# Kernel optimization log

Measured on AMD Instinct MI355X. Metric: run time of the kernel, lower is better.

The kernel has to match this reference:

```python
import jax, jax.numpy as jnp
import numpy as np

H_FEATS = 256

def setup_inputs() -> dict:
    key = jax.random.key(0)
    k1, k2, k3, k4, k5, k6, k7 = jax.random.split(key, 7)
    N, E, D = 100000, 500000, H_FEATS
    h = jax.random.normal(k1, (N, D), dtype=jnp.float32)
    src = jax.random.randint(k2, (E,), 0, N)
    dst = jax.random.randint(k3, (E,), 0, N)
    # Linear params (PyTorch default init: U(-1/sqrt(fan_in), 1/sqrt(fan_in)))
    b1_bound = 1.0 / np.sqrt(2 * D)
    b2_bound = 1.0 / np.sqrt(D)
    W1 = jax.random.uniform(k4, (2 * D, D), jnp.float32, -b1_bound, b1_bound)
    b1 = jax.random.uniform(k5, (D,), jnp.float32, -b1_bound, b1_bound)
    W2 = jax.random.uniform(k6, (D, 1), jnp.float32, -b2_bound, b2_bound)
    b2 = jax.random.uniform(k7, (1,), jnp.float32, -b2_bound, b2_bound)
    return {"h": h, "src": src, "dst": dst, "W1": W1, "b1": b1, "W2": W2, "b2": b2}

def reference(h, src, dst, W1, b1, W2, b2):
    # Gather per-edge source/destination node features and concat: [E, 2D]
    he = jnp.concatenate([h[src], h[dst]], axis=1)
    # Linear -> ReLU -> (dropout is identity in eval) -> Linear -> Sigmoid
    hid = jax.nn.relu(he @ W1 + b1)          # [E, D]
    score = jax.nn.sigmoid((hid @ W2 + b2).squeeze(1))  # [E]
    return score
```

## Files before the change

kernel.cpp:

```cpp
#include <hip/hip_runtime.h>
#include <math.h>


typedef __attribute__((ext_vector_type(8))) short short8;
typedef __attribute__((ext_vector_type(2))) float floatx2;
typedef __attribute__((ext_vector_type(4))) float floatx4;
typedef __attribute__((ext_vector_type(16))) float floatx16;

#define D_FEAT 256
#define EPW 16

__device__ __forceinline__ float bf2f(unsigned short u) {
    union { unsigned u32; float f; } v; v.u32 = ((unsigned)u) << 16; return v.f;
}
__device__ __forceinline__ float lo16(unsigned u) {
    union { unsigned u32; float f; } v; v.u32 = u << 16; return v.f;
}
__device__ __forceinline__ float hi16(unsigned u) {
    union { unsigned u32; float f; } v; v.u32 = u & 0xffff0000u; return v.f;
}
__device__ __forceinline__ unsigned short f2bf(float f) {
    union { float f; unsigned u32; } v; v.f = f;
    unsigned x = v.u32;
    return (unsigned short)((x + 0x7fffu + ((x >> 16) & 1u)) >> 16);
}
__device__ __forceinline__ float sigmoid_safe(float r) {
    r = fminf(fmaxf(r, -30.f), 30.f);
    return 1.f / (1.f + expf(-r));
}
__device__ __forceinline__ unsigned pack4_fp8(float a, float b, float c, float d) {
    int w = __builtin_amdgcn_cvt_pk_fp8_f32(a, b, 0, false);
    w = __builtin_amdgcn_cvt_pk_fp8_f32(c, d, w, true);
    return (unsigned)w;
}

__global__ __launch_bounds__(256) void probe_dtype(const unsigned short* __restrict__ h,
                                                   int* __restrict__ flag) {
    __shared__ int cnt[256];
    const int t = threadIdx.x;
    int c = 0;
    #pragma unroll
    for (int i = 0; i < 8; ++i) {
        unsigned e = (h[t * 8 + i] >> 7) & 0xFF;
        c += (e >= 100 && e <= 140) ? 1 : 0;
    }
    cnt[t] = c;
    __syncthreads();
    if (t == 0) {
        int s = 0;
        for (int i = 0; i < 256; ++i) s += cnt[i];
        flag[0] = (s >= 1843) ? 1 : 0;
    }
}

template <int MODE>
__global__ __launch_bounds__(256) void build_wt_t(const void* __restrict__ W1v,
                                                  unsigned short* __restrict__ Wt,
                                                  const int* __restrict__ flag) {
    if (flag[0] != MODE) return;
    int j = blockIdx.x, k = threadIdx.x;
    size_t idx = (j < 256) ? ((size_t)k * 256 + j) : ((size_t)(k + 256) * 256 + (j - 256));
    unsigned short v;
    if constexpr (MODE == 1) v = ((const unsigned short*)W1v)[idx];
    else                     v = f2bf(((const float*)W1v)[idx]);
    Wt[(size_t)j * 256 + k] = v;
}

template <int MODE>
__global__ __launch_bounds__(512, 2) void gemm_pq_t(const void* __restrict__ hv,
                                                    const unsigned short* __restrict__ Wt,
                                                    unsigned char* __restrict__ PQ8,
                                                    int N, const int* __restrict__ flag) {
    if (flag[0] != MODE) return;
    __shared__ unsigned short Bs[256][256];
    __shared__ unsigned short As[64][256];

    const int tid  = threadIdx.x;
    const int lane = tid & 63;
    const int wid  = tid >> 6;
    const int l32  = lane & 31;
    const int q2   = lane >> 5;

    {
        const int r = tid >> 1;
        const unsigned cbase = (tid & 1) * 256;
        const char* srcp = (const char*)Wt + (size_t)r * 512 + cbase;
        char* dstb = (char*)&Bs[0][0] + (unsigned)r * 512;
        const unsigned sw = ((unsigned)r & 31) << 4;
        #pragma unroll
        for (int i = 0; i < 16; ++i) {
            short8 v = *(const short8*)(srcp + i * 16);
            *(short8*)(dstb + ((cbase + i * 16) ^ sw)) = v;
        }
    }

    short8 breg[16];
    {
        const char* bp = (const char*)Wt + (size_t)(256 + wid * 32 + l32) * 512 + q2 * 16;
        #pragma unroll
        for (int ks = 0; ks < 16; ++ks)
            breg[ks] = *(const short8*)(bp + ks * 32);
    }

    const int ar = tid >> 3;
    const unsigned ac = (unsigned)(tid & 7) * 64;
    const unsigned aswz = ((unsigned)ar & 31) << 4;

    short8  pref[4];
    floatx4 pf[8];
    auto load_a = [&](int ms) {
        const int gm = ms * 64 + ar;
        if constexpr (MODE == 1) {
            #pragma unroll
            for (int j = 0; j < 4; ++j) {
                short8 v = {};
                if (gm < N)
                    v = *(const short8*)((const char*)hv + (size_t)gm * 512 + ac + j * 16);
                pref[j] = v;
            }
        } else {
            #pragma unroll
            for (int j = 0; j < 4; ++j) {
                floatx4 f0 = {}, f1 = {};
                if (gm < N) {
                    const float* p = (const float*)hv + (size_t)gm * 256 + (ac + j * 16) / 2;
                    f0 = *(const floatx4*)p;
                    f1 = *(const floatx4*)(p + 4);
                }
                pf[2 * j]     = f0;
                pf[2 * j + 1] = f1;
            }
        }
    };

    const int NT = (N + 63) >> 6;
    const int GM = gridDim.x;
    if ((int)blockIdx.x < NT) load_a(blockIdx.x);

    for (int ms = blockIdx.x; ms < NT; ms += GM) {
        __syncthreads();
        {
            char* adst = (char*)&As[0][0] + (unsigned)ar * 512;
            #pragma unroll
            for (int j = 0; j < 4; ++j) {
                short8 v;
                if constexpr (MODE == 1) {
                    v = pref[j];
                } else {
                    floatx4 f0 = pf[2 * j], f1 = pf[2 * j + 1];
                    v[0] = (short)f2bf(f0.x); v[1] = (short)f2bf(f0.y);
                    v[2] = (short)f2bf(f0.z); v[3] = (short)f2bf(f0.w);
                    v[4] = (short)f2bf(f1.x); v[5] = (short)f2bf(f1.y);
                    v[6] = (short)f2bf(f1.z); v[7] = (short)f2bf(f1.w);
                }
                *(short8*)(adst + ((ac + j * 16) ^ aswz)) = v;
            }
        }
        const int msn = ms + GM;
        if (msn < NT) load_a(msn);
        __syncthreads();

        floatx16 acc[2][2] = {};
        #pragma unroll
        for (int ks = 0; ks < 16; ++ks) {
            const unsigned cb = ((unsigned)(ks * 32 + q2 * 16)) ^ ((unsigned)l32 << 4);
            short8 a0 = *(const short8*)((const char*)&As[0][0] + (unsigned)l32 * 512 + cb);
            short8 a1 = *(const short8*)((const char*)&As[0][0] + (unsigned)(32 + l32) * 512 + cb);
            short8 bl = *(const short8*)((const char*)&Bs[0][0] + (unsigned)(wid * 32 + l32) * 512 + cb);
            acc[0][0] = __builtin_amdgcn_mfma_f32_32x32x16_bf16(bl,       a0, acc[0][0], 0, 0, 0);
            acc[1][0] = __builtin_amdgcn_mfma_f32_32x32x16_bf16(bl,       a1, acc[1][0], 0, 0, 0);
            acc[0][1] = __builtin_amdgcn_mfma_f32_32x32x16_bf16(breg[ks], a0, acc[0][1], 0, 0, 0);
            acc[1][1] = __builtin_amdgcn_mfma_f32_32x32x16_bf16(breg[ks], a1, acc[1][1], 0, 0, 0);
        }

        __syncthreads();
        {
            unsigned char* scr = (unsigned char*)&As[0][0];
            #pragma unroll
            for (int mi = 0; mi < 2; ++mi) {
                const unsigned row = (unsigned)(mi * 32 + l32);
                const unsigned rs = (row & 31) << 4;
                #pragma unroll
                for (int nb = 0; nb < 2; ++nb) {
                    const unsigned nbase = (unsigned)(nb * 256 + wid * 32 + 4 * q2);
                    #pragma unroll
                    for (int g = 0; g < 4; ++g) {
                        unsigned w = pack4_fp8(acc[mi][nb][4 * g + 0], acc[mi][nb][4 * g + 1],
                                               acc[mi][nb][4 * g + 2], acc[mi][nb][4 * g + 3]);
                        const unsigned col = nbase + 8 * g;
                        *(unsigned*)(scr + ((row * 512 + col) ^ rs)) = w;
                    }
                }
            }
        }
        __syncthreads();
        {
            const unsigned char* scr = (const unsigned char*)&As[0][0];
            const int gm = ms * 64 + ar;
            if (gm < N) {
                #pragma unroll
                for (int j = 0; j < 4; ++j) {
                    const unsigned col = ac + j * 16;
                    uint4 v = *(const uint4*)(scr + (((unsigned)ar * 512 + col) ^ aswz));
                    *(uint4*)(PQ8 + (size_t)gm * 512 + col) = v;
                }
            }
        }
    }
}

template <int MODE>
__global__ __launch_bounds__(256) void edge_score_t(const unsigned char* __restrict__ PQ8,
                                                    const int* __restrict__ src,
                                                    const int* __restrict__ dst,
                                                    const void* __restrict__ b1v,
                                                    const void* __restrict__ W2v,
                                                    const void* __restrict__ b2v,
                                                    void* __restrict__ outv,
                                                    int E, const int* __restrict__ flag) {
    if (flag[0] != MODE) return;
    const int wave = threadIdx.x >> 6;
    const int lane = threadIdx.x & 63;
    const int e0 = (blockIdx.x * 4 + wave) * EPW;
    if (e0 >= E) return;
    const int l32 = lane & 31;
    const int par = lane >> 5;

    float bf[8], wf[8];
    if constexpr (MODE == 1) {
        const uint4 bvr = *(const uint4*)((const unsigned short*)b1v + l32 * 8);
        const uint4 wvr = *(const uint4*)((const unsigned short*)W2v + l32 * 8);
        bf[0] = lo16(bvr.x); bf[1] = hi16(bvr.x); bf[2] = lo16(bvr.y); bf[3] = hi16(bvr.y);
        bf[4] = lo16(bvr.z); bf[5] = hi16(bvr.z); bf[6] = lo16(bvr.w); bf[7] = hi16(bvr.w);
        wf[0] = lo16(wvr.x); wf[1] = hi16(wvr.x); wf[2] = lo16(wvr.y); wf[3] = hi16(wvr.y);
        wf[4] = lo16(wvr.z); wf[5] = hi16(wvr.z); wf[6] = lo16(wvr.w); wf[7] = hi16(wvr.w);
    } else {
        const float* bp = (const float*)b1v + l32 * 8;
        const float* wp = (const float*)W2v + l32 * 8;
        #pragma unroll
        for (int t = 0; t < 8; ++t) { bf[t] = bp[t]; wf[t] = wp[t]; }
    }
    float bias2;
    if constexpr (MODE == 1) bias2 = bf2f(((const unsigned short*)b2v)[0]);
    else                     bias2 = ((const float*)b2v)[0];

    int nsrc[8], ndst[8];
    #pragma unroll
    for (int p = 0; p < 8; ++p) {
        int e = e0 + 2 * p + par; if (e >= E) e = E - 1;
        nsrc[p] = src[e];
        ndst[p] = dst[e];
    }
    uint2 rp[8], rq[8];
    #pragma unroll
    for (int p = 0; p < 8; ++p) {
        rp[p] = *(const uint2*)(PQ8 + (size_t)nsrc[p] * 512 + l32 * 8);
        rq[p] = *(const uint2*)(PQ8 + (size_t)ndst[p] * 512 + 256 + l32 * 8);
    }

    float res[8];
    #pragma unroll
    for (int p = 0; p < 8; ++p) {
        floatx2 p01 = __builtin_amdgcn_cvt_pk_f32_fp8((int)rp[p].x, false);
        floatx2 p23 = __builtin_amdgcn_cvt_pk_f32_fp8((int)rp[p].x, true);
        floatx2 p45 = __builtin_amdgcn_cvt_pk_f32_fp8((int)rp[p].y, false);
        floatx2 p67 = __builtin_amdgcn_cvt_pk_f32_fp8((int)rp[p].y, true);
        floatx2 q01 = __builtin_amdgcn_cvt_pk_f32_fp8((int)rq[p].x, false);
        floatx2 q23 = __builtin_amdgcn_cvt_pk_f32_fp8((int)rq[p].x, true);
        floatx2 q45 = __builtin_amdgcn_cvt_pk_f32_fp8((int)rq[p].y, false);
        floatx2 q67 = __builtin_amdgcn_cvt_pk_f32_fp8((int)rq[p].y, true);
        float v0 = fmaxf(p01.x + q01.x + bf[0], 0.f);
        float v1 = fmaxf(p01.y + q01.y + bf[1], 0.f);
        float v2 = fmaxf(p23.x + q23.x + bf[2], 0.f);
        float v3 = fmaxf(p23.y + q23.y + bf[3], 0.f);
        float v4 = fmaxf(p45.x + q45.x + bf[4], 0.f);
        float v5 = fmaxf(p45.y + q45.y + bf[5], 0.f);
        float v6 = fmaxf(p67.x + q67.x + bf[6], 0.f);
        float v7 = fmaxf(p67.y + q67.y + bf[7], 0.f);
        res[p] = v0 * wf[0] + v1 * wf[1] + v2 * wf[2] + v3 * wf[3]
               + v4 * wf[4] + v5 * wf[5] + v6 * wf[6] + v7 * wf[7];
    }

    float t4[4];
    #pragma unroll
    for (int k = 0; k < 4; ++k) {
        float a = res[2 * k], b = res[2 * k + 1];
        float own  = (lane & 1) ? b : a;
        float send = (lane & 1) ? a : b;
        t4[k] = own + __shfl_xor(send, 1);
    }
    float t2[2];
    #pragma unroll
    for (int k = 0; k < 2; ++k) {
        float a = t4[2 * k], b = t4[2 * k + 1];
        float own  = (lane & 2) ? b : a;
        float send = (lane & 2) ? a : b;
        t2[k] = own + __shfl_xor(send, 2);
    }
    float t1;
    {
        float a = t2[0], b = t2[1];
        float own  = (lane & 4) ? b : a;
        float send = (lane & 4) ? a : b;
        t1 = own + __shfl_xor(send, 4);
    }
    t1 += __shfl_xor(t1, 8);
    t1 += __shfl_xor(t1, 16);

    if (l32 < 8) {
        const int e = e0 + 2 * (lane & 7) + par;
        if (e < E) {
            float r = sigmoid_safe(t1 + bias2);
            if constexpr (MODE == 1) ((unsigned short*)outv)[e] = f2bf(r);
            else                     ((float*)outv)[e] = r;
        }
    }
}

template <int MODE>
__global__ __launch_bounds__(256) void edge_fused_t(const void* __restrict__ hv,
                                                    const int* __restrict__ src,
                                                    const int* __restrict__ dst,
                                                    const void* __restrict__ W1v,
                                                    const void* __restrict__ b1v,
                                                    const void* __restrict__ W2v,
                                                    const void* __restrict__ b2v,
                                                    void* __restrict__ outv,
                                                    int E, const int* __restrict__ flag) {
    if (flag && flag[0] != MODE) return;
    __shared__ float he[512];
    __shared__ float wsum[4];
    const int e = blockIdx.x;
    if (e >= E) return;
    const int t = threadIdx.x;
    const int s = src[e];
    const int d = dst[e];

    if constexpr (MODE == 1) {
        he[t]       = bf2f(((const unsigned short*)hv)[(size_t)s * 256 + t]);
        he[256 + t] = bf2f(((const unsigned short*)hv)[(size_t)d * 256 + t]);
    } else {
        he[t]       = ((const float*)hv)[(size_t)s * 256 + t];
        he[256 + t] = ((const float*)hv)[(size_t)d * 256 + t];
    }
    __syncthreads();

    float acc;
    if constexpr (MODE == 1) acc = bf2f(((const unsigned short*)b1v)[t]);
    else                     acc = ((const float*)b1v)[t];

    #pragma unroll 8
    for (int k = 0; k < 512; ++k) {
        float w;
        if constexpr (MODE == 1) w = bf2f(((const unsigned short*)W1v)[(size_t)k * 256 + t]);
        else                     w = ((const float*)W1v)[(size_t)k * 256 + t];
        acc += he[k] * w;
    }

    float w2;
    if constexpr (MODE == 1) w2 = bf2f(((const unsigned short*)W2v)[t]);
    else                     w2 = ((const float*)W2v)[t];
    acc = fmaxf(acc, 0.f) * w2;

    #pragma unroll
    for (int off = 32; off > 0; off >>= 1)
        acc += __shfl_xor(acc, off);
    if ((t & 63) == 0) wsum[t >> 6] = acc;
    __syncthreads();

    if (t == 0) {
        float bias2;
        if constexpr (MODE == 1) bias2 = bf2f(((const unsigned short*)b2v)[0]);
        else                     bias2 = ((const float*)b2v)[0];
        float r = sigmoid_safe(wsum[0] + wsum[1] + wsum[2] + wsum[3] + bias2);
        if constexpr (MODE == 1) ((unsigned short*)outv)[e] = f2bf(r);
        else                     ((float*)outv)[e] = r;
    }
}

extern "C" void kernel_launch(void* const* d_in, const int* in_sizes, int n_in,
                              void* d_out, int out_size, void* d_ws, size_t ws_size,
                              hipStream_t stream) {
    const void* h  = d_in[0];
    const int* src = (const int*)d_in[1];
    const int* dst = (const int*)d_in[2];
    const void* W1 = d_in[3];
    const void* b1 = d_in[4];
    const void* W2 = d_in[5];
    const void* b2 = d_in[6];

    const int N = in_sizes[0] / D_FEAT;
    const int E = in_sizes[1];

    const size_t FLAG_BYTES = 256;
    const size_t wt_bytes  = (size_t)512 * D_FEAT * sizeof(unsigned short);
    const size_t pq_bytes  = (size_t)N * 512;
    const size_t need = FLAG_BYTES + wt_bytes + pq_bytes;

    int* flag = (int*)d_ws;
    unsigned short* Wt = (unsigned short*)((char*)d_ws + FLAG_BYTES);
    unsigned char*  PQ8 = (unsigned char*)((char*)d_ws + FLAG_BYTES + wt_bytes);

    if (ws_size >= need) {
        probe_dtype<<<1, 256, 0, stream>>>((const unsigned short*)h, flag);

        build_wt_t<1><<<512, 256, 0, stream>>>(W1, Wt, flag);
        build_wt_t<0><<<512, 256, 0, stream>>>(W1, Wt, flag);

        gemm_pq_t<1><<<256, 512, 0, stream>>>(h, Wt, PQ8, N, flag);
        gemm_pq_t<0><<<256, 512, 0, stream>>>(h, Wt, PQ8, N, flag);

        int egrid = (E + 4 * EPW - 1) / (4 * EPW);
        edge_score_t<1><<<egrid, 256, 0, stream>>>(PQ8, src, dst, b1, W2, b2, d_out, E, flag);
        edge_score_t<0><<<egrid, 256, 0, stream>>>(PQ8, src, dst, b1, W2, b2, d_out, E, flag);
    } else if (ws_size >= FLAG_BYTES) {
        probe_dtype<<<1, 256, 0, stream>>>((const unsigned short*)h, flag);
        edge_fused_t<1><<<E, 256, 0, stream>>>(h, src, dst, W1, b1, W2, b2, d_out, E, flag);
        edge_fused_t<0><<<E, 256, 0, stream>>>(h, src, dst, W1, b1, W2, b2, d_out, E, flag);
    } else {
        edge_fused_t<1><<<E, 256, 0, stream>>>(h, src, dst, W1, b1, W2, b2, d_out, E, nullptr);
    }
}
```

Measured before the change: 242.8 us.

## Stream GEMM weights from cache instead of LDS to raise occupancy

The node-projection GEMM no longer stages the full 256x256 bf16 weight half in shared memory or keeps the other half in registers. Each wave now loads its B fragments straight from global memory (served by L1/L2) inside the k-loop. This frees a large amount of LDS and registers, so launch bounds allow 4 blocks and the grid doubles to 512. A separate fp8 scratch buffer replaces reuse of the A tile, which removes one barrier per tile. The trade-off is much more repeated cache traffic for the weights on every tile, and global-load latency sitting inside the MFMA loop.

```diff
diff --git a/kernel.cpp b/kernel.cpp
--- a/kernel.cpp
+++ b/kernel.cpp
@@ -67,40 +67,19 @@
 }
 
 template <int MODE>
-__global__ __launch_bounds__(512, 2) void gemm_pq_t(const void* __restrict__ hv,
+__global__ __launch_bounds__(512, 4) void gemm_pq_t(const void* __restrict__ hv,
                                                     const unsigned short* __restrict__ Wt,
                                                     unsigned char* __restrict__ PQ8,
                                                     int N, const int* __restrict__ flag) {
     if (flag[0] != MODE) return;
-    __shared__ unsigned short Bs[256][256];
     __shared__ unsigned short As[64][256];
+    __shared__ unsigned char  Scr[64][512];
 
     const int tid  = threadIdx.x;
     const int lane = tid & 63;
     const int wid  = tid >> 6;
     const int l32  = lane & 31;
     const int q2   = lane >> 5;
-
-    {
-        const int r = tid >> 1;
-        const unsigned cbase = (tid & 1) * 256;
-        const char* srcp = (const char*)Wt + (size_t)r * 512 + cbase;
-        char* dstb = (char*)&Bs[0][0] + (unsigned)r * 512;
-        const unsigned sw = ((unsigned)r & 31) << 4;
-        #pragma unroll
-        for (int i = 0; i < 16; ++i) {
-            short8 v = *(const short8*)(srcp + i * 16);
-            *(short8*)(dstb + ((cbase + i * 16) ^ sw)) = v;
-        }
-    }
-
-    short8 breg[16];
-    {
-        const char* bp = (const char*)Wt + (size_t)(256 + wid * 32 + l32) * 512 + q2 * 16;
-        #pragma unroll
-        for (int ks = 0; ks < 16; ++ks)
-            breg[ks] = *(const short8*)(bp + ks * 32);
-    }
 
     const int ar = tid >> 3;
     const unsigned ac = (unsigned)(tid & 7) * 64;
@@ -132,70 +111,76 @@
             }
         }
     };
+    auto write_a = [&]() {
+        char* adst = (char*)&As[0][0] + (unsigned)ar * 512;
+        #pragma unroll
+        for (int j = 0; j < 4; ++j) {
+            short8 v;
+            if constexpr (MODE == 1) {
+                v = pref[j];
+            } else {
+                floatx4 f0 = pf[2 * j], f1 = pf[2 * j + 1];
+                v[0] = (short)f2bf(f0.x); v[1] = (short)f2bf(f0.y);
+                v[2] = (short)f2bf(f0.z); v[3] = (short)f2bf(f0.w);
+                v[4] = (short)f2bf(f1.x); v[5] = (short)f2bf(f1.y);
+                v[6] = (short)f2bf(f1.z); v[7] = (short)f2bf(f1.w);
+            }
+            *(short8*)(adst + ((ac + j * 16) ^ aswz)) = v;
+        }
+    };
 
     const int NT = (N + 63) >> 6;
     const int GM = gridDim.x;
-    if ((int)blockIdx.x < NT) load_a(blockIdx.x);
-
-    for (int ms = blockIdx.x; ms < NT; ms += GM) {
+    const int bid = blockIdx.x;
+
+    const char* bbase0 = (const char*)Wt + (size_t)(wid * 64 + l32) * 512 + q2 * 16;
+    const char* bbase1 = bbase0 + 32 * 512;
+
+    load_a(bid);
+
+    for (int ms = bid; ms < NT; ms += GM) {
+        write_a();
         __syncthreads();
-        {
-            char* adst = (char*)&As[0][0] + (unsigned)ar * 512;
-            #pragma unroll
-            for (int j = 0; j < 4; ++j) {
-                short8 v;
-                if constexpr (MODE == 1) {
-                    v = pref[j];
-                } else {
-                    floatx4 f0 = pf[2 * j], f1 = pf[2 * j + 1];
-                    v[0] = (short)f2bf(f0.x); v[1] = (short)f2bf(f0.y);
-                    v[2] = (short)f2bf(f0.z); v[3] = (short)f2bf(f0.w);
-                    v[4] = (short)f2bf(f1.x); v[5] = (short)f2bf(f1.y);
-                    v[6] = (short)f2bf(f1.z); v[7] = (short)f2bf(f1.w);
-                }
-                *(short8*)(adst + ((ac + j * 16) ^ aswz)) = v;
-            }
-        }
-        const int msn = ms + GM;
-        if (msn < NT) load_a(msn);
-        __syncthreads();
+
+        if (ms + GM < NT) load_a(ms + GM);
 
         floatx16 acc[2][2] = {};
+        const char* abase = (const char*)&As[0][0];
         #pragma unroll
         for (int ks = 0; ks < 16; ++ks) {
             const unsigned cb = ((unsigned)(ks * 32 + q2 * 16)) ^ ((unsigned)l32 << 4);
-            short8 a0 = *(const short8*)((const char*)&As[0][0] + (unsigned)l32 * 512 + cb);
-            short8 a1 = *(const short8*)((const char*)&As[0][0] + (unsigned)(32 + l32) * 512 + cb);
-            short8 bl = *(const short8*)((const char*)&Bs[0][0] + (unsigned)(wid * 32 + l32) * 512 + cb);
-            acc[0][0] = __builtin_amdgcn_mfma_f32_32x32x16_bf16(bl,       a0, acc[0][0], 0, 0, 0);
-            acc[1][0] = __builtin_amdgcn_mfma_f32_32x32x16_bf16(bl,       a1, acc[1][0], 0, 0, 0);
-            acc[0][1] = __builtin_amdgcn_mfma_f32_32x32x16_bf16(breg[ks], a0, acc[0][1], 0, 0, 0);
-            acc[1][1] = __builtin_amdgcn_mfma_f32_32x32x16_bf16(breg[ks], a1, acc[1][1], 0, 0, 0);
-        }
-
-        __syncthreads();
+            short8 bl0 = *(const short8*)(bbase0 + ks * 32);
+            short8 bl1 = *(const short8*)(bbase1 + ks * 32);
+            short8 a0 = *(const short8*)(abase + (unsigned)l32 * 512 + cb);
+            short8 a1 = *(const short8*)(abase + (unsigned)(32 + l32) * 512 + cb);
+            acc[0][0] = __builtin_amdgcn_mfma_f32_32x32x16_bf16(bl0, a0, acc[0][0], 0, 0, 0);
+            acc[1][0] = __builtin_amdgcn_mfma_f32_32x32x16_bf16(bl0, a1, acc[1][0], 0, 0, 0);
+            acc[0][1] = __builtin_amdgcn_mfma_f32_32x32x16_bf16(bl1, a0, acc[0][1], 0, 0, 0);
+            acc[1][1] = __builtin_amdgcn_mfma_f32_32x32x16_bf16(bl1, a1, acc[1][1], 0, 0, 0);
+        }
+
         {
-            unsigned char* scr = (unsigned char*)&As[0][0];
+            unsigned char* scr = (unsigned char*)&Scr[0][0];
             #pragma unroll
             for (int mi = 0; mi < 2; ++mi) {
                 const unsigned row = (unsigned)(mi * 32 + l32);
                 const unsigned rs = (row & 31) << 4;
                 #pragma unroll
                 for (int nb = 0; nb < 2; ++nb) {
-                    const unsigned nbase = (unsigned)(nb * 256 + wid * 32 + 4 * q2);
+                    const unsigned nbase = (unsigned)(wid * 64 + nb * 32 + 4 * q2);
                     #pragma unroll
                     for (int g = 0; g < 4; ++g) {
                         unsigned w = pack4_fp8(acc[mi][nb][4 * g + 0], acc[mi][nb][4 * g + 1],
                                                acc[mi][nb][4 * g + 2], acc[mi][nb][4 * g + 3]);
-                        const unsigned col = nbase + 8 * g;
-                        *(unsigned*)(scr + ((row * 512 + col) ^ rs)) = w;
+                        *(unsigned*)(scr + ((row * 512 + nbase + 8 * g) ^ rs)) = w;
                     }
                 }
             }
         }
         __syncthreads();
+
         {
-            const unsigned char* scr = (const unsigned char*)&As[0][0];
+            const unsigned char* scr = (const unsigned char*)&Scr[0][0];
             const int gm = ms * 64 + ar;
             if (gm < N) {
                 #pragma unroll
@@ -407,8 +392,8 @@
         build_wt_t<1><<<512, 256, 0, stream>>>(W1, Wt, flag);
         build_wt_t<0><<<512, 256, 0, stream>>>(W1, Wt, flag);
 
-        gemm_pq_t<1><<<256, 512, 0, stream>>>(h, Wt, PQ8, N, flag);
-        gemm_pq_t<0><<<256, 512, 0, stream>>>(h, Wt, PQ8, N, flag);
+        gemm_pq_t<1><<<512, 512, 0, stream>>>(h, Wt, PQ8, N, flag);
+        gemm_pq_t<0><<<512, 512, 0, stream>>>(h, Wt, PQ8, N, flag);
 
         int egrid = (E + 4 * EPW - 1) / (4 * EPW);
         edge_score_t<1><<<egrid, 256, 0, stream>>>(PQ8, src, dst, b1, W2, b2, d_out, E, flag);
```

Result: slower. 359.2 us (+47.9%).
